# Kernel optimization log

Hardware: AMD Instinct MI355X
Metric: run time of the kernel (lower is better)

Reference implementation:

```python
import jax, jax.numpy as jnp
import numpy as np

K = 1024
H = 16

def setup_inputs() -> dict:
    key = jax.random.key(0)
    ks = jax.random.split(key, 6)
    s = 1.0 / np.sqrt(K)
    return {
        "x": jax.random.normal(ks[0], (2, 2048, K), dtype=jnp.float32),
        "Wq": jax.random.uniform(ks[1], (K, K), jnp.float32, -s, s),
        "Wk": jax.random.uniform(ks[2], (K, K), jnp.float32, -s, s),
        "Wv": jax.random.uniform(ks[3], (K, K), jnp.float32, -s, s),
        "Wu": jax.random.uniform(ks[4], (K, K), jnp.float32, -s, s),
        "bu": jax.random.uniform(ks[5], (K,), jnp.float32, -s, s),
    }

def reference(x, Wq, Wk, Wv, Wu, bu):
    b, t, k = x.shape
    hd = k // H  # head dim = 64
    scale = jnp.asarray(k, x.dtype) ** 0.25  # Bloem-style: scale q and k each by k^(1/4)
    # nn.Linear(bias=False): y = x @ W.T
    q = (jnp.einsum('btk,ok->bto', x, Wq) / scale).reshape(b, t, H, hd)
    kk = (jnp.einsum('btk,ok->bto', x, Wk) / scale).reshape(b, t, H, hd)
    v = jnp.einsum('btk,ok->bto', x, Wv).reshape(b, t, H, hd)
    dot = jnp.einsum('bthd,bshd->bhts', q, kk)  # [b,h,t,t]
    att = jax.nn.softmax(dot, axis=-1)
    out = jnp.einsum('bhts,bshd->bthd', att, v).reshape(b, t, k)
    return jnp.einsum('btk,ok->bto', out, Wu) + bu
```

## Files before the change

kernel.cpp:

```cpp
#include <hip/hip_runtime.h>

typedef __bf16 bf16;
typedef bf16  bf16x8 __attribute__((ext_vector_type(8)));
typedef bf16  bf16x4 __attribute__((ext_vector_type(4)));
typedef float f32x4  __attribute__((ext_vector_type(4)));

#define MFMA16(a, b, c) __builtin_amdgcn_mfma_f32_16x16x32_bf16((a), (b), (c), 0, 0, 0)
#define AS1 __attribute__((address_space(1)))
#define AS3 __attribute__((address_space(3)))

__device__ __forceinline__ void gld_lds16(const bf16* g, bf16* l) {
    __builtin_amdgcn_global_load_lds((AS1 void*)(g), (AS3 void*)(l), 16, 0, 0);
}


__global__ __launch_bounds__(256) void cvt_all(const float* __restrict__ x,
                                               const float* __restrict__ Wq, const float* __restrict__ Wk,
                                               const float* __restrict__ Wv, const float* __restrict__ Wu,
                                               bf16* ox, bf16* oq, bf16* ok, bf16* ov, bf16* ou,
                                               float sq, float sk) {
    int bid = blockIdx.x;
    const float* src; bf16* dst; float sc; int base;
    if (bid < 4096) { src = x; dst = ox; sc = 1.0f; base = bid; }
    else {
        int w = (bid - 4096) >> 10; base = (bid - 4096) & 1023;
        switch (w) {
            case 0:  src = Wq; dst = oq; sc = sq;   break;
            case 1:  src = Wk; dst = ok; sc = sk;   break;
            case 2:  src = Wv; dst = ov; sc = 1.0f; break;
            default: src = Wu; dst = ou; sc = 1.0f; break;
        }
    }
    int idx = (base * 256 + threadIdx.x) * 4;
    float4 v = *(const float4*)(src + idx);
    bf16x4 o;
    o[0] = (bf16)(v.x * sc); o[1] = (bf16)(v.y * sc);
    o[2] = (bf16)(v.z * sc); o[3] = (bf16)(v.w * sc);
    *(bf16x4*)(dst + idx) = o;
}

__device__ __forceinline__ void gemm_core(const bf16* __restrict__ A, const bf16* __restrict__ B,
                                          int mBase, int nBase, bf16* As, bf16* Bs,
                                          f32x4 acc[4][4]) {
    const int tid = threadIdx.x;
    const int wave = tid >> 6, lane = tid & 63;
    const int g = lane >> 4, lr = lane & 15;
    const int wm = (wave & 1) << 6, wn = (wave >> 1) << 6;
    const int q = lane >> 2;
    const int cswz = ((lane & 3) ^ ((lane >> 3) & 3)) << 3;
    const int pcs  = (g ^ ((lr >> 1) & 3)) << 3;

    const int rb0 = wave << 4, rb1 = rb0 + 64;
    const bf16* a0 = A + (size_t)(mBase + rb0 + q) * 1024 + cswz;
    const bf16* a1 = A + (size_t)(mBase + rb1 + q) * 1024 + cswz;
    const bf16* b0 = B + (size_t)(nBase + rb0 + q) * 1024 + cswz;
    const bf16* b1 = B + (size_t)(nBase + rb1 + q) * 1024 + cswz;

    for (int k0 = 0; k0 < 1024; k0 += 32) {
        __syncthreads();
        gld_lds16(a0 + k0, As + rb0 * 32);
        gld_lds16(a1 + k0, As + rb1 * 32);
        gld_lds16(b0 + k0, Bs + rb0 * 32);
        gld_lds16(b1 + k0, Bs + rb1 * 32);
        __syncthreads();

        bf16x8 af[4], bfr[4];
#pragma unroll
        for (int i = 0; i < 4; i++)
            af[i] = *(const bf16x8*)&As[(wm + (i << 4) + lr) * 32 + pcs];
#pragma unroll
        for (int j = 0; j < 4; j++)
            bfr[j] = *(const bf16x8*)&Bs[(wn + (j << 4) + lr) * 32 + pcs];
#pragma unroll
        for (int i = 0; i < 4; i++)
#pragma unroll
            for (int j = 0; j < 4; j++)
                acc[i][j] = MFMA16(af[i], bfr[j], acc[i][j]);
    }
}

__global__ __launch_bounds__(256) void gemm_qkv(const bf16* __restrict__ X,
                                                const bf16* __restrict__ Wqk,
                                                const bf16* __restrict__ Wv,
                                                bf16* __restrict__ Qo, bf16* __restrict__ Ko,
                                                bf16* __restrict__ Vto) {
    __shared__ bf16 As[128 * 32];
    __shared__ bf16 Bs[128 * 32];
    const int tid = threadIdx.x;
    const int wave = tid >> 6, lane = tid & 63;
    const int g = lane >> 4, lr = lane & 15;
    const int wm = (wave & 1) << 6, wn = (wave >> 1) << 6;
    const int my = blockIdx.y;
    const bool qk = (my < 16);

    const bf16* Ap = qk ? Wqk : X;
    const bf16* Bp = qk ? X   : Wv;
    const int mBase = qk ? my * 128 : blockIdx.x * 128;
    const int nBase = qk ? blockIdx.x * 128 : (my - 16) * 128;

    f32x4 acc[4][4] = {};
    gemm_core(Ap, Bp, mBase, nBase, As, Bs, acc);

    if (qk) {
#pragma unroll
        for (int i = 0; i < 4; i++) {
            int m0 = mBase + wm + (i << 4) + (g << 2);
            bf16* dst = (m0 >> 10) ? Ko : Qo;
            int feat = m0 & 1023;
            int h = feat >> 6, d = feat & 63;
#pragma unroll
            for (int j = 0; j < 4; j++) {
                int t = nBase + wn + (j << 4) + lr;
                int b = t >> 11, tl = t & 2047;
                bf16x4 v;
#pragma unroll
                for (int r = 0; r < 4; r++) v[r] = (bf16)acc[i][j][r];
                *(bf16x4*)&dst[(((size_t)((b << 4) + h) * 2048 + tl) << 6) + d] = v;
            }
        }
    } else {
#pragma unroll
        for (int i = 0; i < 4; i++) {
            int t0 = mBase + wm + (i << 4) + (g << 2);
            int b = t0 >> 11, tl = t0 & 2047;
#pragma unroll
            for (int j = 0; j < 4; j++) {
                int o = nBase + wn + (j << 4) + lr;
                int h = o >> 6, d = o & 63;
                bf16x4 v;
#pragma unroll
                for (int r = 0; r < 4; r++) v[r] = (bf16)acc[i][j][r];
                *(bf16x4*)&Vto[((size_t)(((b << 4) + h) << 6) + d) * 2048 + tl] = v;
            }
        }
    }
}

__global__ __launch_bounds__(256) void gemm_out(const bf16* __restrict__ Wu, const bf16* __restrict__ A,
                                                const float* __restrict__ bias, float* __restrict__ out) {
    __shared__ bf16 As[128 * 32];
    __shared__ bf16 Bs[128 * 32];
    const int tid = threadIdx.x;
    const int wave = tid >> 6, lane = tid & 63;
    const int g = lane >> 4, lr = lane & 15;
    const int wm = (wave & 1) << 6, wn = (wave >> 1) << 6;
    const int mBase = blockIdx.y * 128, nBase = blockIdx.x * 128;

    f32x4 acc[4][4] = {};
    gemm_core(Wu, A, mBase, nBase, As, Bs, acc);

#pragma unroll
    for (int i = 0; i < 4; i++) {
        int o = mBase + wm + (i << 4) + (g << 2);
        float4 bv = *(const float4*)&bias[o];
#pragma unroll
        for (int j = 0; j < 4; j++) {
            int t = nBase + wn + (j << 4) + lr;
            float4 v;
            v.x = acc[i][j][0] + bv.x;
            v.y = acc[i][j][1] + bv.y;
            v.z = acc[i][j][2] + bv.z;
            v.w = acc[i][j][3] + bv.w;
            *(float4*)&out[((size_t)t << 10) + o] = v;
        }
    }
}

__global__ __launch_bounds__(256, 4) void attn(const bf16* __restrict__ Q, const bf16* __restrict__ Kt,
                                               const bf16* __restrict__ Vt, bf16* __restrict__ O) {
    __shared__ bf16 Qs[2][64][32];
    __shared__ bf16 Ks[2][128][32];
    __shared__ bf16 Vs[4][64][32];
    bf16 (*Ps)[16][32] = (bf16(*)[16][32]) & Qs[0][0][0];

    const int tid = threadIdx.x;
    const int wave = tid >> 6, lane = tid & 63;
    const int g = lane >> 4, lr = lane & 15;
    const int q = lane >> 2;
    const int cswz = ((lane & 3) ^ ((lane >> 3) & 3)) << 3;
    const int pcs  = (g ^ ((lr >> 1) & 3)) << 3;
    const int pw0 = ((((g >> 1))     ^ ((lr >> 1) & 3)) << 3) + ((g & 1) << 2);
    const int pw1 = (((2 + (g >> 1)) ^ ((lr >> 1) & 3)) << 3) + ((g & 1) << 2);

    const int bid = blockIdx.x;
    const int bh = ((bid & 7) << 2) | (bid >> 8);
    const int qt = (bid >> 3) & 31;
    const int qBase = qt << 6;

    const bf16* Qg = Q + ((size_t)bh * 2048 + qBase) * 64;
    const bf16* Kg = Kt + (size_t)bh * 2048 * 64;
    const bf16* Vg = Vt + (size_t)bh * 64 * 2048;

#pragma unroll
    for (int i = 0; i < 2; i++) {
        int bi = (wave << 1) + i;
        int p = bi >> 2, rb = (bi & 3) << 4;
        gld_lds16(Qg + (rb + q) * 64 + (p << 5) + cswz, &Qs[p][rb][0]);
    }
    __syncthreads();

    bf16x8 qf[2];
#pragma unroll
    for (int ks = 0; ks < 2; ks++)
        qf[ks] = *(const bf16x8*)&Qs[ks][(wave << 4) + lr][pcs];

    bf16x8 ones;
#pragma unroll
    for (int i = 0; i < 8; i++) ones[i] = (bf16)1.0f;

    f32x4 oacc[4] = {};
    f32x4 oaccL = {};

    for (int s0 = 0; s0 < 2048; s0 += 128) {
        __syncthreads();
#pragma unroll
        for (int i = 0; i < 4; i++) {
            int bi = (wave << 2) + i;
            {
                int p = bi >> 3, rb = (bi & 7) << 4;
                gld_lds16(Kg + (size_t)(s0 + rb + q) * 64 + (p << 5) + cswz, &Ks[p][rb][0]);
            }
            {
                int p = bi >> 2, rb = (bi & 3) << 4;
                gld_lds16(Vg + (size_t)(rb + q) * 2048 + s0 + (p << 5) + cswz, &Vs[p][rb][0]);
            }
        }
        __syncthreads();

#pragma unroll
        for (int ks2 = 0; ks2 < 4; ks2++) {
            f32x4 sacc[2] = {};
#pragma unroll
            for (int isub = 0; isub < 2; isub++) {
                int is = (ks2 << 1) + isub;
#pragma unroll
                for (int ks = 0; ks < 2; ks++) {
                    bf16x8 kf = *(const bf16x8*)&Ks[ks][(is << 4) + lr][pcs];
                    sacc[isub] = MFMA16(kf, qf[ks], sacc[isub]);
                }
            }
#pragma unroll
            for (int isub = 0; isub < 2; isub++) {
                f32x4 s = sacc[isub];
                bf16x4 pb;
                pb[0] = (bf16)__builtin_amdgcn_exp2f(s[0]);
                pb[1] = (bf16)__builtin_amdgcn_exp2f(s[1]);
                pb[2] = (bf16)__builtin_amdgcn_exp2f(s[2]);
                pb[3] = (bf16)__builtin_amdgcn_exp2f(s[3]);
                *(bf16x4*)&Ps[wave][lr][isub ? pw1 : pw0] = pb;
            }
            bf16x8 pf = *(const bf16x8*)&Ps[wave][lr][pcs];
#pragma unroll
            for (int jd = 0; jd < 4; jd++) {
                bf16x8 vf = *(const bf16x8*)&Vs[ks2][(jd << 4) + lr][pcs];
                oacc[jd] = MFMA16(pf, vf, oacc[jd]);
            }
            oaccL = MFMA16(pf, ones, oaccL);
        }
    }

    float linv[4];
#pragma unroll
    for (int r = 0; r < 4; r++) linv[r] = 1.0f / oaccL[r];

    const int b = bh >> 4, h = bh & 15;
#pragma unroll
    for (int jd = 0; jd < 4; jd++)
#pragma unroll
        for (int r = 0; r < 4; r++) {
            int t = qBase + (wave << 4) + (g << 2) + r;
            int col = (h << 6) + (jd << 4) + lr;
            O[(((size_t)(b * 2048 + t)) << 10) + col] = (bf16)(oacc[jd][r] * linv[r]);
        }
}

extern "C" void kernel_launch(void* const* d_in, const int* in_sizes, int n_in,
                              void* d_out, int out_size, void* d_ws, size_t ws_size,
                              hipStream_t stream) {
    const float* x  = (const float*)d_in[0];
    const float* Wq = (const float*)d_in[1];
    const float* Wk = (const float*)d_in[2];
    const float* Wv = (const float*)d_in[3];
    const float* Wu = (const float*)d_in[4];
    const float* bu = (const float*)d_in[5];
    float* out = (float*)d_out;

    char* ws = (char*)d_ws;
    bf16* xbf  = (bf16*)(ws);
    bf16* wqbf = (bf16*)(ws + ((size_t)8  << 20));
    bf16* wkbf = (bf16*)(ws + ((size_t)10 << 20));
    bf16* wvbf = (bf16*)(ws + ((size_t)12 << 20));
    bf16* wubf = (bf16*)(ws + ((size_t)14 << 20));
    bf16* Qb   = (bf16*)(ws + ((size_t)16 << 20));
    bf16* Kb   = (bf16*)(ws + ((size_t)24 << 20));
    bf16* Vtb  = (bf16*)(ws + ((size_t)32 << 20));
    bf16* attnO = xbf;

    const float iscale_k = 0.17677669529663687f;
    const float iscale_q = 0.25503540109f;

    cvt_all<<<8192, 256, 0, stream>>>(x, Wq, Wk, Wv, Wu, xbf, wqbf, wkbf, wvbf, wubf,
                                      iscale_q, iscale_k);

    gemm_qkv<<<dim3(32, 24), 256, 0, stream>>>(xbf, wqbf, wvbf, Qb, Kb, Vtb);
    attn<<<dim3(1024), 256, 0, stream>>>(Qb, Kb, Vtb, attnO);
    gemm_out<<<dim3(32, 8), 256, 0, stream>>>(wubf, attnO, bu, out);
}
```

Baseline: 190.6 us.

## Repartition attention waves: split S over keys, PV over query/dim quadrants

The attention kernel now has each wave compute scores for a 32-key slice across all 64 queries, writing exp'd probabilities into a shared 64x128 P tile. In the PV phase each wave owns a 32-query by 32-dim quadrant. Q and V fragments are read straight from global memory instead of being staged in LDS, and the row sums are accumulated in registers and reduced across waves through LDS rather than computed by an extra MFMA against a ones vector. The aim is to cut the redundant MFMA and shared-memory traffic. In exchange it adds a block-wide barrier per key tile between the S and PV phases, plus uncoalesced direct global loads of V.

```diff
diff --git a/kernel.cpp b/kernel.cpp
--- a/kernel.cpp
+++ b/kernel.cpp
@@ -168,10 +168,9 @@
 
 __global__ __launch_bounds__(256, 4) void attn(const bf16* __restrict__ Q, const bf16* __restrict__ Kt,
                                                const bf16* __restrict__ Vt, bf16* __restrict__ O) {
-    __shared__ bf16 Qs[2][64][32];
     __shared__ bf16 Ks[2][128][32];
-    __shared__ bf16 Vs[4][64][32];
-    bf16 (*Ps)[16][32] = (bf16(*)[16][32]) & Qs[0][0][0];
+    __shared__ bf16 Ps[64][128];
+    float* Lbuf = (float*)&Ks[0][0][0];
 
     const int tid = threadIdx.x;
     const int wave = tid >> 6, lane = tid & 63;
@@ -179,99 +178,117 @@
     const int q = lane >> 2;
     const int cswz = ((lane & 3) ^ ((lane >> 3) & 3)) << 3;
     const int pcs  = (g ^ ((lr >> 1) & 3)) << 3;
-    const int pw0 = ((((g >> 1))     ^ ((lr >> 1) & 3)) << 3) + ((g & 1) << 2);
-    const int pw1 = (((2 + (g >> 1)) ^ ((lr >> 1) & 3)) << 3) + ((g & 1) << 2);
+    const int lr7  = lr & 7;
+    const int thalf = wave >> 1, dhalf = wave & 1;
 
     const int bid = blockIdx.x;
     const int bh = ((bid & 7) << 2) | (bid >> 8);
-    const int qt = (bid >> 3) & 31;
-    const int qBase = qt << 6;
+    const int qBase = ((bid >> 3) & 31) << 6;
 
     const bf16* Qg = Q + ((size_t)bh * 2048 + qBase) * 64;
     const bf16* Kg = Kt + (size_t)bh * 2048 * 64;
     const bf16* Vg = Vt + (size_t)bh * 64 * 2048;
 
-#pragma unroll
-    for (int i = 0; i < 2; i++) {
-        int bi = (wave << 1) + i;
-        int p = bi >> 2, rb = (bi & 3) << 4;
-        gld_lds16(Qg + (rb + q) * 64 + (p << 5) + cswz, &Qs[p][rb][0]);
-    }
-    __syncthreads();
-
-    bf16x8 qf[2];
+    bf16x8 qf[2][4];
 #pragma unroll
     for (int ks = 0; ks < 2; ks++)
-        qf[ks] = *(const bf16x8*)&Qs[ks][(wave << 4) + lr][pcs];
-
-    bf16x8 ones;
-#pragma unroll
-    for (int i = 0; i < 8; i++) ones[i] = (bf16)1.0f;
-
-    f32x4 oacc[4] = {};
-    f32x4 oaccL = {};
+#pragma unroll
+        for (int tt = 0; tt < 4; tt++)
+            qf[ks][tt] = *(const bf16x8*)(Qg + ((tt << 4) + lr) * 64 + (ks << 5) + (g << 3));
+
+    const int pw0 = ((((wave << 2) + (g >> 1))     ^ lr7) << 3) + ((g & 1) << 2);
+    const int pw1 = ((((wave << 2) + 2 + (g >> 1)) ^ lr7) << 3) + ((g & 1) << 2);
+
+    f32x4 oacc[2][2] = {};
+    f32x4 lsumv[4] = {};
 
     for (int s0 = 0; s0 < 2048; s0 += 128) {
         __syncthreads();
 #pragma unroll
         for (int i = 0; i < 4; i++) {
             int bi = (wave << 2) + i;
-            {
-                int p = bi >> 3, rb = (bi & 7) << 4;
-                gld_lds16(Kg + (size_t)(s0 + rb + q) * 64 + (p << 5) + cswz, &Ks[p][rb][0]);
-            }
-            {
-                int p = bi >> 2, rb = (bi & 3) << 4;
-                gld_lds16(Vg + (size_t)(rb + q) * 2048 + s0 + (p << 5) + cswz, &Vs[p][rb][0]);
+            int p = bi >> 3, rb = (bi & 7) << 4;
+            gld_lds16(Kg + (size_t)(s0 + rb + q) * 64 + (p << 5) + cswz, &Ks[p][rb][0]);
+        }
+        __syncthreads();
+
+#pragma unroll
+        for (int isub = 0; isub < 2; isub++) {
+            f32x4 sacc[4] = {};
+#pragma unroll
+            for (int ks = 0; ks < 2; ks++) {
+                bf16x8 kf = *(const bf16x8*)&Ks[ks][(wave << 5) + (isub << 4) + lr][pcs];
+#pragma unroll
+                for (int tt = 0; tt < 4; tt++)
+                    sacc[tt] = MFMA16(kf, qf[ks][tt], sacc[tt]);
+            }
+#pragma unroll
+            for (int tt = 0; tt < 4; tt++) {
+                f32x4 e;
+                e[0] = __builtin_amdgcn_exp2f(sacc[tt][0]);
+                e[1] = __builtin_amdgcn_exp2f(sacc[tt][1]);
+                e[2] = __builtin_amdgcn_exp2f(sacc[tt][2]);
+                e[3] = __builtin_amdgcn_exp2f(sacc[tt][3]);
+                lsumv[tt] += e;
+                bf16x4 pb;
+                pb[0] = (bf16)e[0]; pb[1] = (bf16)e[1]; pb[2] = (bf16)e[2]; pb[3] = (bf16)e[3];
+                *(bf16x4*)&Ps[(tt << 4) + lr][isub ? pw1 : pw0] = pb;
             }
         }
         __syncthreads();
 
 #pragma unroll
         for (int ks2 = 0; ks2 < 4; ks2++) {
-            f32x4 sacc[2] = {};
-#pragma unroll
-            for (int isub = 0; isub < 2; isub++) {
-                int is = (ks2 << 1) + isub;
-#pragma unroll
-                for (int ks = 0; ks < 2; ks++) {
-                    bf16x8 kf = *(const bf16x8*)&Ks[ks][(is << 4) + lr][pcs];
-                    sacc[isub] = MFMA16(kf, qf[ks], sacc[isub]);
-                }
-            }
-#pragma unroll
-            for (int isub = 0; isub < 2; isub++) {
-                f32x4 s = sacc[isub];
-                bf16x4 pb;
-                pb[0] = (bf16)__builtin_amdgcn_exp2f(s[0]);
-                pb[1] = (bf16)__builtin_amdgcn_exp2f(s[1]);
-                pb[2] = (bf16)__builtin_amdgcn_exp2f(s[2]);
-                pb[3] = (bf16)__builtin_amdgcn_exp2f(s[3]);
-                *(bf16x4*)&Ps[wave][lr][isub ? pw1 : pw0] = pb;
-            }
-            bf16x8 pf = *(const bf16x8*)&Ps[wave][lr][pcs];
-#pragma unroll
-            for (int jd = 0; jd < 4; jd++) {
-                bf16x8 vf = *(const bf16x8*)&Vs[ks2][(jd << 4) + lr][pcs];
-                oacc[jd] = MFMA16(pf, vf, oacc[jd]);
-            }
-            oaccL = MFMA16(pf, ones, oaccL);
-        }
-    }
-
-    float linv[4];
-#pragma unroll
-    for (int r = 0; r < 4; r++) linv[r] = 1.0f / oaccL[r];
+            bf16x8 vf[2], pf[2];
+#pragma unroll
+            for (int dd = 0; dd < 2; dd++)
+                vf[dd] = *(const bf16x8*)(Vg + (size_t)((dhalf << 5) + (dd << 4) + lr) * 2048
+                                          + s0 + (ks2 << 5) + (g << 3));
+#pragma unroll
+            for (int tt = 0; tt < 2; tt++)
+                pf[tt] = *(const bf16x8*)&Ps[(thalf << 5) + (tt << 4) + lr]
+                                            [(((ks2 << 2) + g) ^ lr7) << 3];
+#pragma unroll
+            for (int tt = 0; tt < 2; tt++)
+#pragma unroll
+                for (int dd = 0; dd < 2; dd++)
+                    oacc[tt][dd] = MFMA16(pf[tt], vf[dd], oacc[tt][dd]);
+        }
+    }
+
+    float lpart[4];
+#pragma unroll
+    for (int tt = 0; tt < 4; tt++) {
+        lpart[tt] = (lsumv[tt][0] + lsumv[tt][1]) + (lsumv[tt][2] + lsumv[tt][3]);
+        lpart[tt] += __shfl_xor(lpart[tt], 16, 64);
+        lpart[tt] += __shfl_xor(lpart[tt], 32, 64);
+    }
+    __syncthreads();
+    if (g == 0) {
+#pragma unroll
+        for (int tt = 0; tt < 4; tt++)
+            Lbuf[(wave << 6) + (tt << 4) + lr] = lpart[tt];
+    }
+    __syncthreads();
 
     const int b = bh >> 4, h = bh & 15;
 #pragma unroll
-    for (int jd = 0; jd < 4; jd++)
+    for (int tt = 0; tt < 2; tt++) {
+        float linv[4];
 #pragma unroll
         for (int r = 0; r < 4; r++) {
-            int t = qBase + (wave << 4) + (g << 2) + r;
-            int col = (h << 6) + (jd << 4) + lr;
-            O[(((size_t)(b * 2048 + t)) << 10) + col] = (bf16)(oacc[jd][r] * linv[r]);
-        }
+            int t = (thalf << 5) + (tt << 4) + (g << 2) + r;
+            linv[r] = 1.0f / (((Lbuf[t] + Lbuf[64 + t]) + (Lbuf[128 + t] + Lbuf[192 + t])));
+        }
+#pragma unroll
+        for (int dd = 0; dd < 2; dd++)
+#pragma unroll
+            for (int r = 0; r < 4; r++) {
+                int t = qBase + (thalf << 5) + (tt << 4) + (g << 2) + r;
+                int col = (h << 6) + (dhalf << 5) + (dd << 4) + lr;
+                O[(((size_t)(b * 2048 + t)) << 10) + col] = (bf16)(oacc[tt][dd][r] * linv[r]);
+            }
+    }
 }
 
 extern "C" void kernel_launch(void* const* d_in, const int* in_sizes, int n_in,
```

Result: slower. 211.1 us (+10.7%).

## Pair attention waves on 32 query rows and split keys between them

Applied to the files above, without the earlier changes.

Waves in the attention kernel are now grouped in pairs. Each pair covers 32 query rows, and the two waves in a pair take opposite halves of every 128-key block. Each K and V fragment read from LDS now feeds two MFMAs instead of one, which cuts shared-memory traffic per FLOP. At the end, the second wave of each pair writes its partial output and row sums to LDS and the first wave combines them. The cost is twice the accumulator registers, one extra barrier with an LDS reduction, and the risk of lower occupancy under the 4-block launch bound.

```diff
diff --git a/kernel.cpp b/kernel.cpp
--- a/kernel.cpp
+++ b/kernel.cpp
@@ -171,7 +171,7 @@
     __shared__ bf16 Qs[2][64][32];
     __shared__ bf16 Ks[2][128][32];
     __shared__ bf16 Vs[4][64][32];
-    bf16 (*Ps)[16][32] = (bf16(*)[16][32]) & Qs[0][0][0];
+    bf16 (*Ps)[32][32] = (bf16(*)[32][32]) & Qs[0][0][0];
 
     const int tid = threadIdx.x;
     const int wave = tid >> 6, lane = tid & 63;
@@ -181,11 +181,12 @@
     const int pcs  = (g ^ ((lr >> 1) & 3)) << 3;
     const int pw0 = ((((g >> 1))     ^ ((lr >> 1) & 3)) << 3) + ((g & 1) << 2);
     const int pw1 = (((2 + (g >> 1)) ^ ((lr >> 1) & 3)) << 3) + ((g & 1) << 2);
+    const int pair = wave >> 1;
+    const int shalf = wave & 1;
 
     const int bid = blockIdx.x;
     const int bh = ((bid & 7) << 2) | (bid >> 8);
-    const int qt = (bid >> 3) & 31;
-    const int qBase = qt << 6;
+    const int qBase = ((bid >> 3) & 31) << 6;
 
     const bf16* Qg = Q + ((size_t)bh * 2048 + qBase) * 64;
     const bf16* Kg = Kt + (size_t)bh * 2048 * 64;
@@ -199,17 +200,19 @@
     }
     __syncthreads();
 
-    bf16x8 qf[2];
+    bf16x8 qf[2][2];
 #pragma unroll
     for (int ks = 0; ks < 2; ks++)
-        qf[ks] = *(const bf16x8*)&Qs[ks][(wave << 4) + lr][pcs];
+#pragma unroll
+        for (int tt = 0; tt < 2; tt++)
+            qf[ks][tt] = *(const bf16x8*)&Qs[ks][(pair << 5) + (tt << 4) + lr][pcs];
 
     bf16x8 ones;
 #pragma unroll
     for (int i = 0; i < 8; i++) ones[i] = (bf16)1.0f;
 
-    f32x4 oacc[4] = {};
-    f32x4 oaccL = {};
+    f32x4 oacc[2][4] = {};
+    f32x4 oaccL[2] = {};
 
     for (int s0 = 0; s0 < 2048; s0 += 128) {
         __syncthreads();
@@ -228,50 +231,77 @@
         __syncthreads();
 
 #pragma unroll
-        for (int ks2 = 0; ks2 < 4; ks2++) {
-            f32x4 sacc[2] = {};
-#pragma unroll
-            for (int isub = 0; isub < 2; isub++) {
-                int is = (ks2 << 1) + isub;
-#pragma unroll
-                for (int ks = 0; ks < 2; ks++) {
-                    bf16x8 kf = *(const bf16x8*)&Ks[ks][(is << 4) + lr][pcs];
-                    sacc[isub] = MFMA16(kf, qf[ks], sacc[isub]);
+        for (int sblk = 0; sblk < 2; sblk++) {
+            f32x4 sacc[2][2] = {};
+#pragma unroll
+            for (int ks = 0; ks < 2; ks++)
+#pragma unroll
+                for (int isub = 0; isub < 2; isub++) {
+                    bf16x8 kf = *(const bf16x8*)
+                        &Ks[ks][(shalf << 6) + (sblk << 5) + (isub << 4) + lr][pcs];
+                    sacc[isub][0] = MFMA16(kf, qf[ks][0], sacc[isub][0]);
+                    sacc[isub][1] = MFMA16(kf, qf[ks][1], sacc[isub][1]);
                 }
-            }
-#pragma unroll
-            for (int isub = 0; isub < 2; isub++) {
-                f32x4 s = sacc[isub];
-                bf16x4 pb;
-                pb[0] = (bf16)__builtin_amdgcn_exp2f(s[0]);
-                pb[1] = (bf16)__builtin_amdgcn_exp2f(s[1]);
-                pb[2] = (bf16)__builtin_amdgcn_exp2f(s[2]);
-                pb[3] = (bf16)__builtin_amdgcn_exp2f(s[3]);
-                *(bf16x4*)&Ps[wave][lr][isub ? pw1 : pw0] = pb;
-            }
-            bf16x8 pf = *(const bf16x8*)&Ps[wave][lr][pcs];
+#pragma unroll
+            for (int isub = 0; isub < 2; isub++)
+#pragma unroll
+                for (int tt = 0; tt < 2; tt++) {
+                    f32x4 s = sacc[isub][tt];
+                    bf16x4 pb;
+                    pb[0] = (bf16)__builtin_amdgcn_exp2f(s[0]);
+                    pb[1] = (bf16)__builtin_amdgcn_exp2f(s[1]);
+                    pb[2] = (bf16)__builtin_amdgcn_exp2f(s[2]);
+                    pb[3] = (bf16)__builtin_amdgcn_exp2f(s[3]);
+                    *(bf16x4*)&Ps[wave][(tt << 4) + lr][isub ? pw1 : pw0] = pb;
+                }
+            bf16x8 pf0 = *(const bf16x8*)&Ps[wave][lr][pcs];
+            bf16x8 pf1 = *(const bf16x8*)&Ps[wave][16 + lr][pcs];
 #pragma unroll
             for (int jd = 0; jd < 4; jd++) {
-                bf16x8 vf = *(const bf16x8*)&Vs[ks2][(jd << 4) + lr][pcs];
-                oacc[jd] = MFMA16(pf, vf, oacc[jd]);
-            }
-            oaccL = MFMA16(pf, ones, oaccL);
-        }
-    }
-
-    float linv[4];
-#pragma unroll
-    for (int r = 0; r < 4; r++) linv[r] = 1.0f / oaccL[r];
-
-    const int b = bh >> 4, h = bh & 15;
-#pragma unroll
-    for (int jd = 0; jd < 4; jd++)
-#pragma unroll
-        for (int r = 0; r < 4; r++) {
-            int t = qBase + (wave << 4) + (g << 2) + r;
-            int col = (h << 6) + (jd << 4) + lr;
-            O[(((size_t)(b * 2048 + t)) << 10) + col] = (bf16)(oacc[jd][r] * linv[r]);
-        }
+                bf16x8 vf = *(const bf16x8*)&Vs[(shalf << 1) + sblk][(jd << 4) + lr][pcs];
+                oacc[0][jd] = MFMA16(pf0, vf, oacc[0][jd]);
+                oacc[1][jd] = MFMA16(pf1, vf, oacc[1][jd]);
+            }
+            oaccL[0] = MFMA16(pf0, ones, oaccL[0]);
+            oaccL[1] = MFMA16(pf1, ones, oaccL[1]);
+        }
+    }
+
+    __syncthreads();
+    float* Odump = (float*)&Ks[0][0][0];
+    float* Ldump = (float*)&Vs[0][0][0];
+    if (shalf == 1) {
+#pragma unroll
+        for (int tt = 0; tt < 2; tt++) {
+#pragma unroll
+            for (int jd = 0; jd < 4; jd++)
+                *(f32x4*)&Odump[(pair << 11) + (((tt << 2) + jd) << 8) + (lane << 2)] = oacc[tt][jd];
+            *(f32x4*)&Ldump[(pair << 9) + (tt << 8) + (lane << 2)] = oaccL[tt];
+        }
+    }
+    __syncthreads();
+    if (shalf == 0) {
+        const int b = bh >> 4, h = bh & 15;
+#pragma unroll
+        for (int tt = 0; tt < 2; tt++) {
+            f32x4 Lp = *(const f32x4*)&Ldump[(pair << 9) + (tt << 8) + (lane << 2)];
+            f32x4 Ls = oaccL[tt] + Lp;
+            float linv[4];
+#pragma unroll
+            for (int r = 0; r < 4; r++) linv[r] = 1.0f / Ls[r];
+#pragma unroll
+            for (int jd = 0; jd < 4; jd++) {
+                f32x4 Op = *(const f32x4*)&Odump[(pair << 11) + (((tt << 2) + jd) << 8) + (lane << 2)];
+                f32x4 v = oacc[tt][jd] + Op;
+#pragma unroll
+                for (int r = 0; r < 4; r++) {
+                    int t = qBase + (pair << 5) + (tt << 4) + (g << 2) + r;
+                    int col = (h << 6) + (jd << 4) + lr;
+                    O[(((size_t)(b * 2048 + t)) << 10) + col] = (bf16)(v[r] * linv[r]);
+                }
+            }
+        }
+    }
 }
 
 extern "C" void kernel_launch(void* const* d_in, const int* in_sizes, int n_in,
```

Result: faster. 184.6 us (-3.1%).
